# Kernel optimization log

Hardware: AMD Instinct MI355X
Metric: run time of the kernel (lower is better)

Reference implementation:

```python
import jax, jax.numpy as jnp
import numpy as np

L, B, D, N = 4096, 4, 1024, 16


def setup_inputs() -> dict:
    key = jax.random.key(0)
    ks = jax.random.split(key, 6)
    x = jax.random.normal(ks[0], (L, B, D), dtype=jnp.float32)
    delta = 0.2 * jax.random.normal(ks[1], (D, N, 1), dtype=jnp.float32)
    alpha = 0.2 * jax.random.normal(ks[2], (D, N, 1), dtype=jnp.float32)
    # beta init: N(0, 0.02) + 1.0 (val is all ones since i % 1 == 0 always)
    beta = 0.02 * jax.random.normal(ks[3], (D, N, 1), dtype=jnp.float32) + 1.0
    gamma = jax.random.normal(ks[4], (D, N), dtype=jnp.float32)
    omega = jax.random.normal(ks[5], (D,), dtype=jnp.float32)
    return {"x": x, "delta": delta, "alpha": alpha, "beta": beta,
            "gamma": gamma, "omega": omega}


def reference(x, delta, alpha, beta, gamma, omega):
    seq_len = x.shape[0]
    scale = (1.0 / gamma.shape[1]) ** 0.5
    # EMA coefficients
    p = jax.nn.sigmoid(delta)                      # (D, N, 1)
    q = 1.0 - p * jax.nn.sigmoid(alpha)            # (D, N, 1)
    # Vandermonde kernel: k[d, l] = sum_n p*beta * q^l * gamma*scale
    t = jnp.arange(seq_len, dtype=x.dtype)         # (L,)
    vander = t[None, None, :] * jnp.log(q)         # (D, N, L)
    kernel = p * beta * jnp.exp(vander)            # (D, N, L)
    k = jnp.einsum('dnl,dn->dl', kernel, gamma * scale)  # (D, L)
    # Residual path
    residual = x * omega                           # (L, B, D)
    # FFT causal convolution along time
    xt = jnp.transpose(x, (1, 2, 0))               # (B, D, L)
    n_fft = 2 * seq_len
    k_f = jnp.fft.rfft(k.astype(jnp.float32), n=n_fft)      # (D, n_fft//2+1)
    x_f = jnp.fft.rfft(xt.astype(jnp.float32), n=n_fft)     # (B, D, n_fft//2+1)
    out = jnp.fft.irfft(x_f * k_f, n=n_fft)[..., :seq_len]  # (B, D, L)
    out = out.astype(x.dtype)
    out = jax.nn.silu(jnp.transpose(out, (2, 0, 1)) + residual)  # (L, B, D)
    return out
```

## Files before the change

kernel.cpp:

```cpp
#include <hip/hip_runtime.h>
#include <math.h>

#define D_SZ 1024
#define CH 4096
#define ROW 4096
#define C_CHUNKS 128
#define LC 32
#define SQ_LC 5

__device__ __forceinline__ void load16(const float* __restrict__ p, int d, float v[16]) {
    const float4* p4 = (const float4*)(p + (size_t)d * 16);
#pragma unroll
    for (int r = 0; r < 4; ++r) {
        float4 t = p4[r];
        v[4*r+0] = t.x; v[4*r+1] = t.y; v[4*r+2] = t.z; v[4*r+3] = t.w;
    }
}

__device__ __forceinline__ void compute_qw(const float* __restrict__ delta,
                                           const float* __restrict__ alpha,
                                           const float* __restrict__ beta,
                                           const float* __restrict__ gamma,
                                           int d, float q[16], float w[16]) {
    float dl[16], al[16], bt[16], gm[16];
    load16(delta, d, dl); load16(alpha, d, al);
    load16(beta, d, bt);  load16(gamma, d, gm);
#pragma unroll
    for (int n = 0; n < 16; ++n) {
        float p  = 1.0f / (1.0f + __expf(-dl[n]));
        float sa = 1.0f / (1.0f + __expf(-al[n]));
        q[n] = 1.0f - p * sa;
        w[n] = p * bt[n] * gm[n] * 0.25f;
    }
}

__device__ __forceinline__ void loadg(const float* __restrict__ xp, int g, float v[8]) {
#pragma unroll
    for (int u = 0; u < 8; ++u) v[u] = xp[(size_t)(g * 8 + u) * ROW];
}

__device__ __forceinline__ void compg(float h[16], const float q[16], const float v[8]) {
#pragma unroll
    for (int u = 0; u < 8; ++u) {
        float xu = v[u];
#pragma unroll
        for (int n = 0; n < 16; ++n) h[n] = fmaf(q[n], h[n], xu);
    }
}

__global__ __launch_bounds__(256) void k_phase1(const float* __restrict__ x,
    float* __restrict__ S,
    const float* __restrict__ delta, const float* __restrict__ alpha,
    const float* __restrict__ beta, const float* __restrict__ gamma) {
    int tid = threadIdx.x;
    int j = blockIdx.x;
    int c = blockIdx.y * 256 + tid;
    int d = c & (D_SZ - 1);
    float q[16], w[16];
    compute_qw(delta, alpha, beta, gamma, d, q, w);
    float h[16];
#pragma unroll
    for (int n = 0; n < 16; ++n) h[n] = 0.0f;
    const float* xp = x + (size_t)j * LC * ROW + c;
    float xa[8], xb[8];
    loadg(xp, 0, xa);
    loadg(xp, 1, xb); compg(h, q, xa);
    loadg(xp, 2, xa); compg(h, q, xb);
    loadg(xp, 3, xb); compg(h, q, xa);
    compg(h, q, xb);
    float4* Sp = (float4*)(S + ((size_t)j * CH + c) * 16);
#pragma unroll
    for (int r = 0; r < 4; ++r)
        Sp[r] = make_float4(h[4*r], h[4*r+1], h[4*r+2], h[4*r+3]);
}

__global__ __launch_bounds__(256) void k_phase2(float* __restrict__ S,
    const float* __restrict__ delta, const float* __restrict__ alpha) {
    int lane = threadIdx.x & 63;
    int wv   = threadIdx.x >> 6;
    int c    = blockIdx.x * 4 + wv;
    int d    = c & (D_SZ - 1);
    float dl[16], al[16];
    load16(delta, d, dl); load16(alpha, d, al);
    float A[16], pw[16];
#pragma unroll
    for (int n = 0; n < 16; ++n) {
        float p  = 1.0f / (1.0f + __expf(-dl[n]));
        float sa = 1.0f / (1.0f + __expf(-al[n]));
        float qn = 1.0f - p * sa;
#pragma unroll
        for (int t = 0; t < SQ_LC; ++t) qn *= qn;
        A[n]  = qn;
        pw[n] = qn * qn;
    }
    float4* Spa = (float4*)(S + ((size_t)(2 * lane)     * CH + c) * 16);
    float4* Spb = (float4*)(S + ((size_t)(2 * lane + 1) * CH + c) * 16);
    float sa16[16], sb16[16];
#pragma unroll
    for (int r = 0; r < 4; ++r) {
        float4 ta = Spa[r], tb = Spb[r];
        sa16[4*r] = ta.x; sa16[4*r+1] = ta.y; sa16[4*r+2] = ta.z; sa16[4*r+3] = ta.w;
        sb16[4*r] = tb.x; sb16[4*r+1] = tb.y; sb16[4*r+2] = tb.z; sb16[4*r+3] = tb.w;
    }
    float hh[16];
#pragma unroll
    for (int n = 0; n < 16; ++n) hh[n] = fmaf(A[n], sa16[n], sb16[n]);
#pragma unroll
    for (int k = 1; k <= 32; k <<= 1) {
        float prev[16];
#pragma unroll
        for (int n = 0; n < 16; ++n) prev[n] = __shfl_up(hh[n], (unsigned)k, 64);
#pragma unroll
        for (int n = 0; n < 16; ++n) hh[n] = (lane >= k) ? fmaf(pw[n], prev[n], hh[n]) : hh[n];
#pragma unroll
        for (int n = 0; n < 16; ++n) pw[n] *= pw[n];
    }
    float Hb[16];
#pragma unroll
    for (int n = 0; n < 16; ++n) {
        float t = __shfl_up(hh[n], 1u, 64);
        Hb[n] = (lane == 0) ? 0.0f : t;
    }
#pragma unroll
    for (int r = 0; r < 4; ++r) {
        Spa[r] = make_float4(Hb[4*r], Hb[4*r+1], Hb[4*r+2], Hb[4*r+3]);
        Spb[r] = make_float4(fmaf(A[4*r],   Hb[4*r],   sa16[4*r]),
                             fmaf(A[4*r+1], Hb[4*r+1], sa16[4*r+1]),
                             fmaf(A[4*r+2], Hb[4*r+2], sa16[4*r+2]),
                             fmaf(A[4*r+3], Hb[4*r+3], sa16[4*r+3]));
    }
}

__device__ __forceinline__ void comp_store(float h[16], const float q[16], const float w[16],
                                           float om, const float v[8],
                                           float* __restrict__ outp, int g) {
#pragma unroll
    for (int u = 0; u < 8; ++u) {
        float xu = v[u];
        float y0 = 0.0f, y1 = 0.0f, y2 = 0.0f, y3 = 0.0f;
#pragma unroll
        for (int n = 0; n < 16; n += 4) {
            h[n]   = fmaf(q[n],   h[n],   xu); y0 = fmaf(w[n],   h[n],   y0);
            h[n+1] = fmaf(q[n+1], h[n+1], xu); y1 = fmaf(w[n+1], h[n+1], y1);
            h[n+2] = fmaf(q[n+2], h[n+2], xu); y2 = fmaf(w[n+2], h[n+2], y2);
            h[n+3] = fmaf(q[n+3], h[n+3], xu); y3 = fmaf(w[n+3], h[n+3], y3);
        }
        float z = (y0 + y1) + (y2 + y3) + xu * om;
        outp[(size_t)(g * 8 + u) * ROW] = z / (1.0f + __expf(-z));
    }
}

__global__ __launch_bounds__(256) void k_phase3(const float* __restrict__ x,
    const float* __restrict__ S, float* __restrict__ out,
    const float* __restrict__ delta, const float* __restrict__ alpha,
    const float* __restrict__ beta, const float* __restrict__ gamma,
    const float* __restrict__ omega) {
    int tid = threadIdx.x;
    int j = blockIdx.x;
    int c = blockIdx.y * 256 + tid;
    int d = c & (D_SZ - 1);
    float q[16], w[16];
    compute_qw(delta, alpha, beta, gamma, d, q, w);
    float om = omega[d];
    float h[16];
    const float4* Sp = (const float4*)(S + ((size_t)j * CH + c) * 16);
#pragma unroll
    for (int r = 0; r < 4; ++r) {
        float4 t = Sp[r];
        h[4*r] = t.x; h[4*r+1] = t.y; h[4*r+2] = t.z; h[4*r+3] = t.w;
    }
    const float* xp = x + (size_t)j * LC * ROW + c;
    float* outp = out + (size_t)j * LC * ROW + c;
    float xa[8], xb[8];
    loadg(xp, 0, xa);
    loadg(xp, 1, xb); comp_store(h, q, w, om, xa, outp, 0);
    loadg(xp, 2, xa); comp_store(h, q, w, om, xb, outp, 1);
    loadg(xp, 3, xb); comp_store(h, q, w, om, xa, outp, 2);
    comp_store(h, q, w, om, xb, outp, 3);
}

extern "C" void kernel_launch(void* const* d_in, const int* in_sizes, int n_in,
                              void* d_out, int out_size, void* d_ws, size_t ws_size,
                              hipStream_t stream) {
    const float* x     = (const float*)d_in[0];
    const float* delta = (const float*)d_in[1];
    const float* alpha = (const float*)d_in[2];
    const float* beta  = (const float*)d_in[3];
    const float* gamma = (const float*)d_in[4];
    const float* omega = (const float*)d_in[5];
    float* out = (float*)d_out;
    float* S   = (float*)d_ws;

    dim3 grid13(C_CHUNKS, CH / 256);
    k_phase1<<<grid13, 256, 0, stream>>>(x, S, delta, alpha, beta, gamma);
    k_phase2<<<CH / 4, 256, 0, stream>>>(S, delta, alpha);
    k_phase3<<<grid13, 256, 0, stream>>>(x, S, out, delta, alpha, beta, gamma, omega);
}
```

Before: 197.6 us.

## Process two channels per thread in scan phases with float2 loads and stores

Phases 1 and 3 now give each thread two adjacent channels, so x and out move through float2 accesses and each block covers 512 channels. The grid axes are swapped so adjacent blocks cover adjacent channels of the same chunk, and launch bounds request 4 blocks per CU. This halves the thread count and widens memory transactions, and gives each thread two independent recurrence chains for more instruction-level parallelism. The cost is doubled register state per thread (32 h, q and w values), which may spill or lower occupancy.

After: 243.9 us. +23.4%, slower.

```diff
diff --git a/kernel.cpp b/kernel.cpp
--- a/kernel.cpp
+++ b/kernel.cpp
@@ -8,25 +8,25 @@
 #define LC 32
 #define SQ_LC 5
 
-__device__ __forceinline__ void load16(const float* __restrict__ p, int d, float v[16]) {
-    const float4* p4 = (const float4*)(p + (size_t)d * 16);
-#pragma unroll
-    for (int r = 0; r < 4; ++r) {
+__device__ __forceinline__ void load32(const float* __restrict__ p, int d0, float v[32]) {
+    const float4* p4 = (const float4*)(p + (size_t)d0 * 16);
+#pragma unroll
+    for (int r = 0; r < 8; ++r) {
         float4 t = p4[r];
         v[4*r+0] = t.x; v[4*r+1] = t.y; v[4*r+2] = t.z; v[4*r+3] = t.w;
     }
 }
 
-__device__ __forceinline__ void compute_qw(const float* __restrict__ delta,
-                                           const float* __restrict__ alpha,
-                                           const float* __restrict__ beta,
-                                           const float* __restrict__ gamma,
-                                           int d, float q[16], float w[16]) {
-    float dl[16], al[16], bt[16], gm[16];
-    load16(delta, d, dl); load16(alpha, d, al);
-    load16(beta, d, bt);  load16(gamma, d, gm);
-#pragma unroll
-    for (int n = 0; n < 16; ++n) {
+__device__ __forceinline__ void compute_qw2(const float* __restrict__ delta,
+                                            const float* __restrict__ alpha,
+                                            const float* __restrict__ beta,
+                                            const float* __restrict__ gamma,
+                                            int d0, float q[32], float w[32]) {
+    float dl[32], al[32], bt[32], gm[32];
+    load32(delta, d0, dl); load32(alpha, d0, al);
+    load32(beta, d0, bt);  load32(gamma, d0, gm);
+#pragma unroll
+    for (int n = 0; n < 32; ++n) {
         float p  = 1.0f / (1.0f + __expf(-dl[n]));
         float sa = 1.0f / (1.0f + __expf(-al[n]));
         q[n] = 1.0f - p * sa;
@@ -34,43 +34,50 @@
     }
 }
 
-__device__ __forceinline__ void loadg(const float* __restrict__ xp, int g, float v[8]) {
-#pragma unroll
-    for (int u = 0; u < 8; ++u) v[u] = xp[(size_t)(g * 8 + u) * ROW];
-}
-
-__device__ __forceinline__ void compg(float h[16], const float q[16], const float v[8]) {
-#pragma unroll
-    for (int u = 0; u < 8; ++u) {
-        float xu = v[u];
-#pragma unroll
-        for (int n = 0; n < 16; ++n) h[n] = fmaf(q[n], h[n], xu);
-    }
-}
-
-__global__ __launch_bounds__(256) void k_phase1(const float* __restrict__ x,
+__device__ __forceinline__ void loadg2(const float* __restrict__ xp, int g, float2 v[4]) {
+#pragma unroll
+    for (int u = 0; u < 4; ++u)
+        v[u] = *(const float2*)(xp + (size_t)(g * 4 + u) * ROW);
+}
+
+__device__ __forceinline__ void compg2(float h[32], const float q[32], const float2 v[4]) {
+#pragma unroll
+    for (int u = 0; u < 4; ++u) {
+        float x0 = v[u].x, x1 = v[u].y;
+#pragma unroll
+        for (int n = 0; n < 16; ++n) h[n]      = fmaf(q[n],      h[n],      x0);
+#pragma unroll
+        for (int n = 0; n < 16; ++n) h[16 + n] = fmaf(q[16 + n], h[16 + n], x1);
+    }
+}
+
+__global__ __launch_bounds__(256, 4) void k_phase1(const float* __restrict__ x,
     float* __restrict__ S,
     const float* __restrict__ delta, const float* __restrict__ alpha,
     const float* __restrict__ beta, const float* __restrict__ gamma) {
-    int tid = threadIdx.x;
-    int j = blockIdx.x;
-    int c = blockIdx.y * 256 + tid;
-    int d = c & (D_SZ - 1);
-    float q[16], w[16];
-    compute_qw(delta, alpha, beta, gamma, d, q, w);
-    float h[16];
-#pragma unroll
-    for (int n = 0; n < 16; ++n) h[n] = 0.0f;
-    const float* xp = x + (size_t)j * LC * ROW + c;
-    float xa[8], xb[8];
-    loadg(xp, 0, xa);
-    loadg(xp, 1, xb); compg(h, q, xa);
-    loadg(xp, 2, xa); compg(h, q, xb);
-    loadg(xp, 3, xb); compg(h, q, xa);
-    compg(h, q, xb);
-    float4* Sp = (float4*)(S + ((size_t)j * CH + c) * 16);
-#pragma unroll
-    for (int r = 0; r < 4; ++r)
+    int t  = threadIdx.x;
+    int j  = blockIdx.y;
+    int c0 = blockIdx.x * 512 + 2 * t;
+    int d0 = c0 & (D_SZ - 1);
+    float q[32], w[32];
+    compute_qw2(delta, alpha, beta, gamma, d0, q, w);
+    float h[32];
+#pragma unroll
+    for (int n = 0; n < 32; ++n) h[n] = 0.0f;
+    const float* xp = x + (size_t)j * LC * ROW + c0;
+    float2 xa[4], xb[4];
+    loadg2(xp, 0, xa);
+    loadg2(xp, 1, xb); compg2(h, q, xa);
+    loadg2(xp, 2, xa); compg2(h, q, xb);
+    loadg2(xp, 3, xb); compg2(h, q, xa);
+    loadg2(xp, 4, xa); compg2(h, q, xb);
+    loadg2(xp, 5, xb); compg2(h, q, xa);
+    loadg2(xp, 6, xa); compg2(h, q, xb);
+    loadg2(xp, 7, xb); compg2(h, q, xa);
+    compg2(h, q, xb);
+    float4* Sp = (float4*)(S + ((size_t)j * CH + c0) * 16);
+#pragma unroll
+    for (int r = 0; r < 8; ++r)
         Sp[r] = make_float4(h[4*r], h[4*r+1], h[4*r+2], h[4*r+3]);
 }
 
@@ -80,18 +87,24 @@
     int wv   = threadIdx.x >> 6;
     int c    = blockIdx.x * 4 + wv;
     int d    = c & (D_SZ - 1);
-    float dl[16], al[16];
-    load16(delta, d, dl); load16(alpha, d, al);
+    const float4* d4 = (const float4*)(delta + (size_t)d * 16);
+    const float4* a4 = (const float4*)(alpha + (size_t)d * 16);
     float A[16], pw[16];
 #pragma unroll
-    for (int n = 0; n < 16; ++n) {
-        float p  = 1.0f / (1.0f + __expf(-dl[n]));
-        float sa = 1.0f / (1.0f + __expf(-al[n]));
-        float qn = 1.0f - p * sa;
-#pragma unroll
-        for (int t = 0; t < SQ_LC; ++t) qn *= qn;
-        A[n]  = qn;
-        pw[n] = qn * qn;
+    for (int r = 0; r < 4; ++r) {
+        float4 td = d4[r], ta = a4[r];
+        float dls[4] = {td.x, td.y, td.z, td.w};
+        float als[4] = {ta.x, ta.y, ta.z, ta.w};
+#pragma unroll
+        for (int k = 0; k < 4; ++k) {
+            float p  = 1.0f / (1.0f + __expf(-dls[k]));
+            float sa = 1.0f / (1.0f + __expf(-als[k]));
+            float qn = 1.0f - p * sa;
+#pragma unroll
+            for (int tq = 0; tq < SQ_LC; ++tq) qn *= qn;
+            A[4*r+k]  = qn;
+            pw[4*r+k] = qn * qn;
+        }
     }
     float4* Spa = (float4*)(S + ((size_t)(2 * lane)     * CH + c) * 16);
     float4* Spb = (float4*)(S + ((size_t)(2 * lane + 1) * CH + c) * 16);
@@ -118,8 +131,8 @@
     float Hb[16];
 #pragma unroll
     for (int n = 0; n < 16; ++n) {
-        float t = __shfl_up(hh[n], 1u, 64);
-        Hb[n] = (lane == 0) ? 0.0f : t;
+        float tv = __shfl_up(hh[n], 1u, 64);
+        Hb[n] = (lane == 0) ? 0.0f : tv;
     }
 #pragma unroll
     for (int r = 0; r < 4; ++r) {
@@ -131,52 +144,63 @@
     }
 }
 
-__device__ __forceinline__ void comp_store(float h[16], const float q[16], const float w[16],
-                                           float om, const float v[8],
-                                           float* __restrict__ outp, int g) {
-#pragma unroll
-    for (int u = 0; u < 8; ++u) {
-        float xu = v[u];
-        float y0 = 0.0f, y1 = 0.0f, y2 = 0.0f, y3 = 0.0f;
-#pragma unroll
-        for (int n = 0; n < 16; n += 4) {
-            h[n]   = fmaf(q[n],   h[n],   xu); y0 = fmaf(w[n],   h[n],   y0);
-            h[n+1] = fmaf(q[n+1], h[n+1], xu); y1 = fmaf(w[n+1], h[n+1], y1);
-            h[n+2] = fmaf(q[n+2], h[n+2], xu); y2 = fmaf(w[n+2], h[n+2], y2);
-            h[n+3] = fmaf(q[n+3], h[n+3], xu); y3 = fmaf(w[n+3], h[n+3], y3);
+__device__ __forceinline__ void comp_store2(float h[32], const float q[32], const float w[32],
+                                            float om0, float om1, const float2 v[4],
+                                            float* __restrict__ outp, int g) {
+#pragma unroll
+    for (int u = 0; u < 4; ++u) {
+        float x0 = v[u].x, x1 = v[u].y;
+        float ya = 0.0f, yb = 0.0f, yc = 0.0f, yd = 0.0f;
+#pragma unroll
+        for (int n = 0; n < 16; n += 2) {
+            h[n]   = fmaf(q[n],   h[n],   x0); ya = fmaf(w[n],   h[n],   ya);
+            h[n+1] = fmaf(q[n+1], h[n+1], x0); yb = fmaf(w[n+1], h[n+1], yb);
         }
-        float z = (y0 + y1) + (y2 + y3) + xu * om;
-        outp[(size_t)(g * 8 + u) * ROW] = z / (1.0f + __expf(-z));
-    }
-}
-
-__global__ __launch_bounds__(256) void k_phase3(const float* __restrict__ x,
+#pragma unroll
+        for (int n = 16; n < 32; n += 2) {
+            h[n]   = fmaf(q[n],   h[n],   x1); yc = fmaf(w[n],   h[n],   yc);
+            h[n+1] = fmaf(q[n+1], h[n+1], x1); yd = fmaf(w[n+1], h[n+1], yd);
+        }
+        float z0 = (ya + yb) + x0 * om0;
+        float z1 = (yc + yd) + x1 * om1;
+        float2 o;
+        o.x = z0 / (1.0f + __expf(-z0));
+        o.y = z1 / (1.0f + __expf(-z1));
+        *(float2*)(outp + (size_t)(g * 4 + u) * ROW) = o;
+    }
+}
+
+__global__ __launch_bounds__(256, 4) void k_phase3(const float* __restrict__ x,
     const float* __restrict__ S, float* __restrict__ out,
     const float* __restrict__ delta, const float* __restrict__ alpha,
     const float* __restrict__ beta, const float* __restrict__ gamma,
     const float* __restrict__ omega) {
-    int tid = threadIdx.x;
-    int j = blockIdx.x;
-    int c = blockIdx.y * 256 + tid;
-    int d = c & (D_SZ - 1);
-    float q[16], w[16];
-    compute_qw(delta, alpha, beta, gamma, d, q, w);
-    float om = omega[d];
-    float h[16];
-    const float4* Sp = (const float4*)(S + ((size_t)j * CH + c) * 16);
-#pragma unroll
-    for (int r = 0; r < 4; ++r) {
-        float4 t = Sp[r];
-        h[4*r] = t.x; h[4*r+1] = t.y; h[4*r+2] = t.z; h[4*r+3] = t.w;
-    }
-    const float* xp = x + (size_t)j * LC * ROW + c;
-    float* outp = out + (size_t)j * LC * ROW + c;
-    float xa[8], xb[8];
-    loadg(xp, 0, xa);
-    loadg(xp, 1, xb); comp_store(h, q, w, om, xa, outp, 0);
-    loadg(xp, 2, xa); comp_store(h, q, w, om, xb, outp, 1);
-    loadg(xp, 3, xb); comp_store(h, q, w, om, xa, outp, 2);
-    comp_store(h, q, w, om, xb, outp, 3);
+    int t  = threadIdx.x;
+    int j  = blockIdx.y;
+    int c0 = blockIdx.x * 512 + 2 * t;
+    int d0 = c0 & (D_SZ - 1);
+    float q[32], w[32];
+    compute_qw2(delta, alpha, beta, gamma, d0, q, w);
+    float2 omv = *(const float2*)(omega + d0);
+    float h[32];
+    const float4* Sp = (const float4*)(S + ((size_t)j * CH + c0) * 16);
+#pragma unroll
+    for (int r = 0; r < 8; ++r) {
+        float4 tv = Sp[r];
+        h[4*r] = tv.x; h[4*r+1] = tv.y; h[4*r+2] = tv.z; h[4*r+3] = tv.w;
+    }
+    const float* xp = x + (size_t)j * LC * ROW + c0;
+    float* outp = out + (size_t)j * LC * ROW + c0;
+    float2 xa[4], xb[4];
+    loadg2(xp, 0, xa);
+    loadg2(xp, 1, xb); comp_store2(h, q, w, omv.x, omv.y, xa, outp, 0);
+    loadg2(xp, 2, xa); comp_store2(h, q, w, omv.x, omv.y, xb, outp, 1);
+    loadg2(xp, 3, xb); comp_store2(h, q, w, omv.x, omv.y, xa, outp, 2);
+    loadg2(xp, 4, xa); comp_store2(h, q, w, omv.x, omv.y, xb, outp, 3);
+    loadg2(xp, 5, xb); comp_store2(h, q, w, omv.x, omv.y, xa, outp, 4);
+    loadg2(xp, 6, xa); comp_store2(h, q, w, omv.x, omv.y, xb, outp, 5);
+    loadg2(xp, 7, xb); comp_store2(h, q, w, omv.x, omv.y, xa, outp, 6);
+    comp_store2(h, q, w, omv.x, omv.y, xb, outp, 7);
 }
 
 extern "C" void kernel_launch(void* const* d_in, const int* in_sizes, int n_in,
@@ -191,7 +215,7 @@
     float* out = (float*)d_out;
     float* S   = (float*)d_ws;
 
-    dim3 grid13(C_CHUNKS, CH / 256);
+    dim3 grid13(CH / 512, C_CHUNKS);
     k_phase1<<<grid13, 256, 0, stream>>>(x, S, delta, alpha, beta, gamma);
     k_phase2<<<CH / 4, 256, 0, stream>>>(S, delta, alpha);
     k_phase3<<<grid13, 256, 0, stream>>>(x, S, out, delta, alpha, beta, gamma, omega);
```

## Split the 16 EMA states across two threads per channel in all phases

Applied to the files above, without the earlier changes.

Each channel's 16 diagonal recurrence states are now split between a pair of adjacent threads, 8 each, doubling the thread count in all three phases. In phase 3 the partial outputs are combined with a lane-xor shuffle, and only one thread of each pair writes the result. The aim is to halve per-thread register pressure and the serial dependency length, raising occupancy and latency hiding. The cost is that both threads of a pair load the same x values, so x reads are duplicated, and half the lanes sit idle during stores.

After: 187.3 us. 1.06x faster.

```diff
diff --git a/kernel.cpp b/kernel.cpp
--- a/kernel.cpp
+++ b/kernel.cpp
@@ -8,25 +8,24 @@
 #define LC 32
 #define SQ_LC 5
 
-__device__ __forceinline__ void load16(const float* __restrict__ p, int d, float v[16]) {
-    const float4* p4 = (const float4*)(p + (size_t)d * 16);
-#pragma unroll
-    for (int r = 0; r < 4; ++r) {
-        float4 t = p4[r];
-        v[4*r+0] = t.x; v[4*r+1] = t.y; v[4*r+2] = t.z; v[4*r+3] = t.w;
-    }
-}
-
-__device__ __forceinline__ void compute_qw(const float* __restrict__ delta,
-                                           const float* __restrict__ alpha,
-                                           const float* __restrict__ beta,
-                                           const float* __restrict__ gamma,
-                                           int d, float q[16], float w[16]) {
-    float dl[16], al[16], bt[16], gm[16];
-    load16(delta, d, dl); load16(alpha, d, al);
-    load16(beta, d, bt);  load16(gamma, d, gm);
-#pragma unroll
-    for (int n = 0; n < 16; ++n) {
+
+__device__ __forceinline__ void load8(const float* __restrict__ p, int d, int m, float v[8]) {
+    const float4* p4 = (const float4*)(p + (size_t)d * 16 + m * 8);
+    float4 a = p4[0], b = p4[1];
+    v[0] = a.x; v[1] = a.y; v[2] = a.z; v[3] = a.w;
+    v[4] = b.x; v[5] = b.y; v[6] = b.z; v[7] = b.w;
+}
+
+__device__ __forceinline__ void compute_qw8(const float* __restrict__ delta,
+                                            const float* __restrict__ alpha,
+                                            const float* __restrict__ beta,
+                                            const float* __restrict__ gamma,
+                                            int d, int m, float q[8], float w[8]) {
+    float dl[8], al[8], bt[8], gm[8];
+    load8(delta, d, m, dl); load8(alpha, d, m, al);
+    load8(beta, d, m, bt);  load8(gamma, d, m, gm);
+#pragma unroll
+    for (int n = 0; n < 8; ++n) {
         float p  = 1.0f / (1.0f + __expf(-dl[n]));
         float sa = 1.0f / (1.0f + __expf(-al[n]));
         q[n] = 1.0f - p * sa;
@@ -39,12 +38,12 @@
     for (int u = 0; u < 8; ++u) v[u] = xp[(size_t)(g * 8 + u) * ROW];
 }
 
-__device__ __forceinline__ void compg(float h[16], const float q[16], const float v[8]) {
+__device__ __forceinline__ void compg8(float h[8], const float q[8], const float v[8]) {
 #pragma unroll
     for (int u = 0; u < 8; ++u) {
         float xu = v[u];
 #pragma unroll
-        for (int n = 0; n < 16; ++n) h[n] = fmaf(q[n], h[n], xu);
+        for (int n = 0; n < 8; ++n) h[n] = fmaf(q[n], h[n], xu);
     }
 }
 
@@ -53,38 +52,41 @@
     const float* __restrict__ delta, const float* __restrict__ alpha,
     const float* __restrict__ beta, const float* __restrict__ gamma) {
     int tid = threadIdx.x;
-    int j = blockIdx.x;
-    int c = blockIdx.y * 256 + tid;
-    int d = c & (D_SZ - 1);
-    float q[16], w[16];
-    compute_qw(delta, alpha, beta, gamma, d, q, w);
-    float h[16];
-#pragma unroll
-    for (int n = 0; n < 16; ++n) h[n] = 0.0f;
+    int j   = blockIdx.x;
+    int pr  = tid >> 1;
+    int m   = tid & 1;
+    int c   = blockIdx.y * 128 + pr;
+    int d   = c & (D_SZ - 1);
+    float q[8], w[8];
+    compute_qw8(delta, alpha, beta, gamma, d, m, q, w);
+    float h[8];
+#pragma unroll
+    for (int n = 0; n < 8; ++n) h[n] = 0.0f;
     const float* xp = x + (size_t)j * LC * ROW + c;
     float xa[8], xb[8];
     loadg(xp, 0, xa);
-    loadg(xp, 1, xb); compg(h, q, xa);
-    loadg(xp, 2, xa); compg(h, q, xb);
-    loadg(xp, 3, xb); compg(h, q, xa);
-    compg(h, q, xb);
-    float4* Sp = (float4*)(S + ((size_t)j * CH + c) * 16);
-#pragma unroll
-    for (int r = 0; r < 4; ++r)
-        Sp[r] = make_float4(h[4*r], h[4*r+1], h[4*r+2], h[4*r+3]);
+    loadg(xp, 1, xb); compg8(h, q, xa);
+    loadg(xp, 2, xa); compg8(h, q, xb);
+    loadg(xp, 3, xb); compg8(h, q, xa);
+    compg8(h, q, xb);
+    float4* Sp = (float4*)(S + ((size_t)j * CH + c) * 16 + m * 8);
+    Sp[0] = make_float4(h[0], h[1], h[2], h[3]);
+    Sp[1] = make_float4(h[4], h[5], h[6], h[7]);
 }
 
 __global__ __launch_bounds__(256) void k_phase2(float* __restrict__ S,
     const float* __restrict__ delta, const float* __restrict__ alpha) {
-    int lane = threadIdx.x & 63;
-    int wv   = threadIdx.x >> 6;
-    int c    = blockIdx.x * 4 + wv;
+    int tid  = threadIdx.x;
+    int wv   = tid >> 6;
+    int lane = tid & 63;
+    int c    = blockIdx.x * 2 + (wv >> 1);
+    int mo   = (wv & 1);
     int d    = c & (D_SZ - 1);
-    float dl[16], al[16];
-    load16(delta, d, dl); load16(alpha, d, al);
-    float A[16], pw[16];
-#pragma unroll
-    for (int n = 0; n < 16; ++n) {
+    float dl[8], al[8];
+    load8(delta, d, mo, dl); load8(alpha, d, mo, al);
+    float A[8], pw[8];
+#pragma unroll
+    for (int n = 0; n < 8; ++n) {
         float p  = 1.0f / (1.0f + __expf(-dl[n]));
         float sa = 1.0f / (1.0f + __expf(-al[n]));
         float qn = 1.0f - p * sa;
@@ -93,60 +95,60 @@
         A[n]  = qn;
         pw[n] = qn * qn;
     }
-    float4* Spa = (float4*)(S + ((size_t)(2 * lane)     * CH + c) * 16);
-    float4* Spb = (float4*)(S + ((size_t)(2 * lane + 1) * CH + c) * 16);
-    float sa16[16], sb16[16];
-#pragma unroll
-    for (int r = 0; r < 4; ++r) {
-        float4 ta = Spa[r], tb = Spb[r];
-        sa16[4*r] = ta.x; sa16[4*r+1] = ta.y; sa16[4*r+2] = ta.z; sa16[4*r+3] = ta.w;
-        sb16[4*r] = tb.x; sb16[4*r+1] = tb.y; sb16[4*r+2] = tb.z; sb16[4*r+3] = tb.w;
-    }
-    float hh[16];
-#pragma unroll
-    for (int n = 0; n < 16; ++n) hh[n] = fmaf(A[n], sa16[n], sb16[n]);
+    float4* Spa = (float4*)(S + ((size_t)(2 * lane)     * CH + c) * 16 + mo * 8);
+    float4* Spb = (float4*)(S + ((size_t)(2 * lane + 1) * CH + c) * 16 + mo * 8);
+    float sa8[8], sb8[8];
+    {
+        float4 a0 = Spa[0], a1 = Spa[1], b0 = Spb[0], b1 = Spb[1];
+        sa8[0]=a0.x; sa8[1]=a0.y; sa8[2]=a0.z; sa8[3]=a0.w;
+        sa8[4]=a1.x; sa8[5]=a1.y; sa8[6]=a1.z; sa8[7]=a1.w;
+        sb8[0]=b0.x; sb8[1]=b0.y; sb8[2]=b0.z; sb8[3]=b0.w;
+        sb8[4]=b1.x; sb8[5]=b1.y; sb8[6]=b1.z; sb8[7]=b1.w;
+    }
+    float hh[8];
+#pragma unroll
+    for (int n = 0; n < 8; ++n) hh[n] = fmaf(A[n], sa8[n], sb8[n]);
 #pragma unroll
     for (int k = 1; k <= 32; k <<= 1) {
-        float prev[16];
-#pragma unroll
-        for (int n = 0; n < 16; ++n) prev[n] = __shfl_up(hh[n], (unsigned)k, 64);
-#pragma unroll
-        for (int n = 0; n < 16; ++n) hh[n] = (lane >= k) ? fmaf(pw[n], prev[n], hh[n]) : hh[n];
-#pragma unroll
-        for (int n = 0; n < 16; ++n) pw[n] *= pw[n];
-    }
-    float Hb[16];
-#pragma unroll
-    for (int n = 0; n < 16; ++n) {
-        float t = __shfl_up(hh[n], 1u, 64);
-        Hb[n] = (lane == 0) ? 0.0f : t;
-    }
-#pragma unroll
-    for (int r = 0; r < 4; ++r) {
-        Spa[r] = make_float4(Hb[4*r], Hb[4*r+1], Hb[4*r+2], Hb[4*r+3]);
-        Spb[r] = make_float4(fmaf(A[4*r],   Hb[4*r],   sa16[4*r]),
-                             fmaf(A[4*r+1], Hb[4*r+1], sa16[4*r+1]),
-                             fmaf(A[4*r+2], Hb[4*r+2], sa16[4*r+2]),
-                             fmaf(A[4*r+3], Hb[4*r+3], sa16[4*r+3]));
-    }
-}
-
-__device__ __forceinline__ void comp_store(float h[16], const float q[16], const float w[16],
-                                           float om, const float v[8],
-                                           float* __restrict__ outp, int g) {
+        float prev[8];
+#pragma unroll
+        for (int n = 0; n < 8; ++n) prev[n] = __shfl_up(hh[n], (unsigned)k, 64);
+#pragma unroll
+        for (int n = 0; n < 8; ++n) hh[n] = (lane >= k) ? fmaf(pw[n], prev[n], hh[n]) : hh[n];
+#pragma unroll
+        for (int n = 0; n < 8; ++n) pw[n] *= pw[n];
+    }
+    float Hb[8];
+#pragma unroll
+    for (int n = 0; n < 8; ++n) {
+        float tv = __shfl_up(hh[n], 1u, 64);
+        Hb[n] = (lane == 0) ? 0.0f : tv;
+    }
+    Spa[0] = make_float4(Hb[0], Hb[1], Hb[2], Hb[3]);
+    Spa[1] = make_float4(Hb[4], Hb[5], Hb[6], Hb[7]);
+    Spb[0] = make_float4(fmaf(A[0], Hb[0], sa8[0]), fmaf(A[1], Hb[1], sa8[1]),
+                         fmaf(A[2], Hb[2], sa8[2]), fmaf(A[3], Hb[3], sa8[3]));
+    Spb[1] = make_float4(fmaf(A[4], Hb[4], sa8[4]), fmaf(A[5], Hb[5], sa8[5]),
+                         fmaf(A[6], Hb[6], sa8[6]), fmaf(A[7], Hb[7], sa8[7]));
+}
+
+__device__ __forceinline__ void comp_store8(float h[8], const float q[8], const float w[8],
+                                            float om, int m, const float v[8],
+                                            float* __restrict__ outp, int g) {
 #pragma unroll
     for (int u = 0; u < 8; ++u) {
         float xu = v[u];
-        float y0 = 0.0f, y1 = 0.0f, y2 = 0.0f, y3 = 0.0f;
-#pragma unroll
-        for (int n = 0; n < 16; n += 4) {
+        float y0 = 0.0f, y1 = 0.0f;
+#pragma unroll
+        for (int n = 0; n < 8; n += 2) {
             h[n]   = fmaf(q[n],   h[n],   xu); y0 = fmaf(w[n],   h[n],   y0);
             h[n+1] = fmaf(q[n+1], h[n+1], xu); y1 = fmaf(w[n+1], h[n+1], y1);
-            h[n+2] = fmaf(q[n+2], h[n+2], xu); y2 = fmaf(w[n+2], h[n+2], y2);
-            h[n+3] = fmaf(q[n+3], h[n+3], xu); y3 = fmaf(w[n+3], h[n+3], y3);
         }
-        float z = (y0 + y1) + (y2 + y3) + xu * om;
-        outp[(size_t)(g * 8 + u) * ROW] = z / (1.0f + __expf(-z));
+        float y  = y0 + y1;
+        float yo = __shfl_xor(y, 1, 64);
+        float z  = y + yo + xu * om;
+        float r  = z / (1.0f + __expf(-z));
+        if (m == 0) outp[(size_t)(g * 8 + u) * ROW] = r;
     }
 }
 
@@ -156,27 +158,29 @@
     const float* __restrict__ beta, const float* __restrict__ gamma,
     const float* __restrict__ omega) {
     int tid = threadIdx.x;
-    int j = blockIdx.x;
-    int c = blockIdx.y * 256 + tid;
-    int d = c & (D_SZ - 1);
-    float q[16], w[16];
-    compute_qw(delta, alpha, beta, gamma, d, q, w);
+    int j   = blockIdx.x;
+    int pr  = tid >> 1;
+    int m   = tid & 1;
+    int c   = blockIdx.y * 128 + pr;
+    int d   = c & (D_SZ - 1);
+    float q[8], w[8];
+    compute_qw8(delta, alpha, beta, gamma, d, m, q, w);
     float om = omega[d];
-    float h[16];
-    const float4* Sp = (const float4*)(S + ((size_t)j * CH + c) * 16);
-#pragma unroll
-    for (int r = 0; r < 4; ++r) {
-        float4 t = Sp[r];
-        h[4*r] = t.x; h[4*r+1] = t.y; h[4*r+2] = t.z; h[4*r+3] = t.w;
-    }
-    const float* xp = x + (size_t)j * LC * ROW + c;
-    float* outp = out + (size_t)j * LC * ROW + c;
+    float h[8];
+    {
+        const float4* Sp = (const float4*)(S + ((size_t)j * CH + c) * 16 + m * 8);
+        float4 a = Sp[0], b = Sp[1];
+        h[0]=a.x; h[1]=a.y; h[2]=a.z; h[3]=a.w;
+        h[4]=b.x; h[5]=b.y; h[6]=b.z; h[7]=b.w;
+    }
+    const float* xp  = x   + (size_t)j * LC * ROW + c;
+    float*       outp = out + (size_t)j * LC * ROW + c;
     float xa[8], xb[8];
     loadg(xp, 0, xa);
-    loadg(xp, 1, xb); comp_store(h, q, w, om, xa, outp, 0);
-    loadg(xp, 2, xa); comp_store(h, q, w, om, xb, outp, 1);
-    loadg(xp, 3, xb); comp_store(h, q, w, om, xa, outp, 2);
-    comp_store(h, q, w, om, xb, outp, 3);
+    loadg(xp, 1, xb); comp_store8(h, q, w, om, m, xa, outp, 0);
+    loadg(xp, 2, xa); comp_store8(h, q, w, om, m, xb, outp, 1);
+    loadg(xp, 3, xb); comp_store8(h, q, w, om, m, xa, outp, 2);
+    comp_store8(h, q, w, om, m, xb, outp, 3);
 }
 
 extern "C" void kernel_launch(void* const* d_in, const int* in_sizes, int n_in,
@@ -191,8 +195,8 @@
     float* out = (float*)d_out;
     float* S   = (float*)d_ws;
 
-    dim3 grid13(C_CHUNKS, CH / 256);
+    dim3 grid13(C_CHUNKS, CH / 128);
     k_phase1<<<grid13, 256, 0, stream>>>(x, S, delta, alpha, beta, gamma);
-    k_phase2<<<CH / 4, 256, 0, stream>>>(S, delta, alpha);
+    k_phase2<<<CH / 2, 256, 0, stream>>>(S, delta, alpha);
     k_phase3<<<grid13, 256, 0, stream>>>(x, S, out, delta, alpha, beta, gamma, omega);
 }
```
